# Optimization experiments

Measured on AMD Instinct MI355X. Metric: run time of the kernel, lower is better.

## Reference

```python
import jax, jax.numpy as jnp
import numpy as np

B, T, N, H, E, K, HOR, OD = 64, 12, 1024, 64, 16, 3, 12, 1
DIN = 1  # input_dim
EPS = 1e-12


def setup_inputs() -> dict:
    key = jax.random.key(0)
    ks = jax.random.split(key, 8)
    s = 0.02
    return {
        "source": jax.random.normal(ks[0], (B, T, N, DIN), jnp.float32),
        "node_emb": jax.random.normal(ks[1], (N, E), jnp.float32),
        "time_emb": jax.random.normal(ks[2], (T, E), jnp.float32),
        "gate_wp": jax.random.normal(ks[3], (E, K, DIN + H, 2 * H), jnp.float32) * s,
        "gate_bp": jax.random.normal(ks[4], (E, 2 * H), jnp.float32) * s,
        "gate_lng": jnp.ones((E,), jnp.float32),
        "gate_lnb": jnp.zeros((E,), jnp.float32),
        "upd_wp": jax.random.normal(ks[5], (E, K, DIN + H, H), jnp.float32) * s,
        "upd_bp": jax.random.normal(ks[6], (E, H), jnp.float32) * s,
        "upd_lng": jnp.ones((E,), jnp.float32),
        "upd_lnb": jnp.zeros((E,), jnp.float32),
        "out_lng": jnp.ones((H,), jnp.float32),
        "out_lnb": jnp.zeros((H,), jnp.float32),
        "conv_w": jax.random.normal(ks[7], (HOR * OD, H), jnp.float32) * s,
        "conv_b": jnp.zeros((HOR * OD,), jnp.float32),
    }


def _ln(x, g, b):
    m = x.mean(-1, keepdims=True)
    v = x.var(-1, keepdims=True)
    return (x - m) / jnp.sqrt(v + EPS) * g + b


def _dagcn(x, node_emb, t_emb, wp, bp, lng, lnb):
    # x: [B, N, C]; node_emb: [N, E]; t_emb: [E] (one timestep)
    e = _ln(node_emb + t_emb[None, :], lng, lnb)          # [N, E] (dropout off in eval)
    sup = jax.nn.softmax(e @ e.T, axis=1)                  # [N, N]
    sl = [jnp.eye(N, dtype=x.dtype), sup]
    for _ in range(2, K):
        sl.append(2.0 * sup @ sl[-1] - sl[-2])             # Chebyshev recursion
    S = jnp.stack(sl, axis=0)                              # [K, N, N]
    w = jnp.einsum('nd,dkio->nkio', e, wp)                 # per-node weights
    bias = e @ bp                                          # [N, O]
    xg = jnp.einsum('knm,bmc->bnkc', S, x)                 # graph conv
    return jnp.einsum('bnki,nkio->bno', xg, w) + bias


def reference(source, node_emb, time_emb, gate_wp, gate_bp, gate_lng, gate_lnb,
              upd_wp, upd_bp, upd_lng, upd_lnb, out_lng, out_lnb, conv_w, conv_b):
    def step(state, xs):
        x_t, te = xs                                        # [B,N,DIN], [E]
        zr = jax.nn.sigmoid(_dagcn(jnp.concatenate([x_t, state], -1),
                                   node_emb, te, gate_wp, gate_bp, gate_lng, gate_lnb))
        z, r = zr[..., :H], zr[..., H:]
        hc = jnp.tanh(_dagcn(jnp.concatenate([x_t, z * state], -1),
                             node_emb, te, upd_wp, upd_bp, upd_lng, upd_lnb))
        h = r * state + (1.0 - r) * hc
        return h, None

    xs = jnp.swapaxes(source, 0, 1)                        # [T,B,N,DIN]
    h0 = jnp.zeros((B, N, H), source.dtype)
    h, _ = jax.lax.scan(step, h0, (xs, time_emb))          # last hidden state [B,N,H]
    y = _ln(h, out_lng, out_lnb)                           # out_dropout off in eval
    out = jnp.einsum('bnh,oh->bon', y, conv_w) + conv_b[None, :, None]  # end_conv
    return out.reshape(B, HOR, OD, N).transpose(0, 1, 3, 2)  # [B,horizon,N,output_dim]
```

## Files before the change

### kernel.cpp

```cpp
#include <hip/hip_runtime.h>
#include <math.h>

namespace {
constexpr int B_ = 64, T_ = 12, N_ = 1024, H_ = 64, E_ = 16;
constexpr int C_  = 65;
constexpr int BC_ = B_ * C_;
constexpr int OG_ = 128;
constexpr int OU_ = 64;
constexpr float EPS_ = 1e-12f;
constexpr int KP_ = 224;
constexpr int COLG_ = OG_ * KP_;
constexpr int COLU_ = OU_ * KP_;
constexpr int NE_ = N_ * E_;
}

typedef unsigned short u16;
typedef unsigned int u32;
using f16x8 = __attribute__((ext_vector_type(8))) _Float16;
using f16x4 = __attribute__((ext_vector_type(4))) _Float16;
using f32x4 = __attribute__((ext_vector_type(4))) float;

__device__ __forceinline__ u32 div65(u32 x) { return (x * 16135u) >> 20; }

__device__ __forceinline__ void gl_lds16(const void* g, void* l, int lane) {
#if __has_builtin(__builtin_amdgcn_global_load_lds)
  __builtin_amdgcn_global_load_lds((const __attribute__((address_space(1))) u32*)g,
                                   (__attribute__((address_space(3))) u32*)l, 16, 0, 0);
#else
  *(uint4*)((char*)l + lane * 16) = *(const uint4*)g;
#endif
}

__device__ __forceinline__ void wprep_body(const float* __restrict__ wp, int NO,
                                           _Float16* __restrict__ wpC, int k, int tid) {
  if (tid >= NO) return;
  f16x8 lo = {}, hi = {};
  if (k < 195) {
    const u32 seg = div65((u32)k);
    const u32 ii = k - seg * 65;
#pragma unroll
    for (int d = 0; d < 8; d++)
      lo[d] = (_Float16)wp[(((size_t)d * 3 + seg) * 65 + ii) * NO + tid];
#pragma unroll
    for (int d = 0; d < 8; d++)
      hi[d] = (_Float16)wp[(((size_t)(d + 8) * 3 + seg) * 65 + ii) * NO + tid];
  }
  _Float16* dst = &wpC[((size_t)tid * KP_ + k) * 16];
  *(f16x8*)dst = lo;
  *(f16x8*)(dst + 8) = hi;
}

__device__ __forceinline__ void sup_body(const float* __restrict__ eT,
                                         _Float16* __restrict__ s16,
                                         int n, int tid, float* red) {
  float en[E_];
#pragma unroll
  for (int d = 0; d < E_; d++) en[d] = eT[d * N_ + n];
  float lg[4];
  float mx = -3.4e38f;
#pragma unroll
  for (int j = 0; j < 4; j++) {
    int m = tid + 256 * j;
    float s = 0.f;
#pragma unroll
    for (int d = 0; d < E_; d++) s = fmaf(en[d], eT[d * N_ + m], s);
    lg[j] = s;
    mx = fmaxf(mx, s);
  }
  red[tid] = mx; __syncthreads();
  for (int off = 128; off > 0; off >>= 1) {
    if (tid < off) red[tid] = fmaxf(red[tid], red[tid + off]);
    __syncthreads();
  }
  mx = red[0]; __syncthreads();
  float sum = 0.f;
#pragma unroll
  for (int j = 0; j < 4; j++) { lg[j] = __expf(lg[j] - mx); sum += lg[j]; }
  red[tid] = sum; __syncthreads();
  for (int off = 128; off > 0; off >>= 1) {
    if (tid < off) red[tid] += red[tid + off];
    __syncthreads();
  }
  float inv = 1.0f / red[0];
#pragma unroll
  for (int j = 0; j < 4; j++)
    s16[(size_t)n * N_ + tid + 256 * j] = (_Float16)(lg[j] * inv);
}

__device__ __forceinline__ void wgen_body(const float* __restrict__ e,
                                          const _Float16* __restrict__ wpC, int COLS,
                                          _Float16* __restrict__ Wt,
                                          int xb, int yb, int tid, float (*es)[16]) {
  const int col0 = xb * 1024 + tid * 4;
  const int n0 = yb * 64;
#pragma unroll
  for (int q = 0; q < 4; q++) {
    int idx = tid + q * 256;
    es[idx >> 4][idx & 15] = e[(size_t)n0 * 16 + idx];
  }
  __syncthreads();
  float wc[4][16];
#pragma unroll
  for (int cc = 0; cc < 4; cc++) {
    f16x8 a = *(const f16x8*)&wpC[(size_t)(col0 + cc) * 16];
    f16x8 b = *(const f16x8*)&wpC[(size_t)(col0 + cc) * 16 + 8];
#pragma unroll
    for (int d = 0; d < 8; d++) { wc[cc][d] = (float)a[d]; wc[cc][8 + d] = (float)b[d]; }
  }
  for (int nn = 0; nn < 64; nn++) {
    float acc[4] = {};
#pragma unroll
    for (int d = 0; d < 16; d++) {
      float ev = es[nn][d];
#pragma unroll
      for (int cc = 0; cc < 4; cc++) acc[cc] = fmaf(ev, wc[cc][d], acc[cc]);
    }
    f16x4 pv;
#pragma unroll
    for (int cc = 0; cc < 4; cc++) pv[cc] = (_Float16)acc[cc];
    *(f16x4*)&Wt[(size_t)(n0 + nn) * COLS + col0] = pv;
  }
}

__device__ __forceinline__ void supT_body(const _Float16* __restrict__ S,
                                          _Float16* __restrict__ ST,
                                          int tile, int tid, _Float16 (*lds)[66]) {
  const int n0 = (tile >> 4) * 64;
  const int m0 = (tile & 15) * 64;
  {
    const int r = tid >> 2, c0 = (tid & 3) * 16;
    const _Float16* sp = &S[(size_t)(n0 + r) * 1024 + m0 + c0];
    f16x8 a = *(const f16x8*)sp;
    f16x8 b = *(const f16x8*)(sp + 8);
#pragma unroll
    for (int i = 0; i < 8; i++) { lds[r][c0 + i] = a[i]; lds[r][c0 + 8 + i] = b[i]; }
  }
  __syncthreads();
  {
    const int c = tid >> 2, r0 = (tid & 3) * 16;
    f16x8 a, b;
#pragma unroll
    for (int i = 0; i < 8; i++) { a[i] = lds[r0 + i][c]; b[i] = lds[r0 + 8 + i][c]; }
    _Float16* dp = &ST[(size_t)(m0 + c) * 1024 + n0 + r0];
    *(f16x8*)dp = a;
    *(f16x8*)(dp + 8) = b;
  }
}

__device__ __forceinline__ void gemm_body(
    const _Float16* __restrict__ A, const _Float16* __restrict__ Bt,
    _Float16* __restrict__ rowout,
    int bx, int by, int tid, _Float16* As, _Float16* Bs) {
  const int wave = tid >> 6, lane = tid & 63;
  const int m0 = by * 128, c0 = bx * 64;
  const int lrow = lane >> 3;
  const int lchunk = lane & 7;
  const int fm = lane & 15, fq = lane >> 4;
  f32x4 acc[2][4] = {};
  for (int ks = 0; ks < 16; ks++) {
    const int kp = ks * 64;
#pragma unroll
    for (int q = 0; q < 4; q++) {
      const int seg = wave * 4 + q;
      const int row = seg * 8 + lrow;
      const int sw = lchunk ^ (row & 7);
      gl_lds16(A + (size_t)(m0 + row) * 1024 + kp + sw * 8, &As[seg * 8 * 64], lane);
    }
#pragma unroll
    for (int q = 0; q < 2; q++) {
      const int seg = wave * 2 + q;
      const int row = seg * 8 + lrow;
      const int sw = lchunk ^ (row & 7);
      gl_lds16(Bt + (size_t)(c0 + row) * 1024 + kp + sw * 8, &Bs[seg * 8 * 64], lane);
    }
    __syncthreads();
#pragma unroll
    for (int kk = 0; kk < 2; kk++) {
      f16x8 af[2], bfr[4];
      const int g = kk * 4 + fq;
#pragma unroll
      for (int mt = 0; mt < 2; mt++) {
        const int row = wave * 32 + mt * 16 + fm;
        af[mt] = *(const f16x8*)&As[row * 64 + (g ^ (row & 7)) * 8];
      }
#pragma unroll
      for (int nt = 0; nt < 4; nt++) {
        const int row = nt * 16 + fm;
        bfr[nt] = *(const f16x8*)&Bs[row * 64 + (g ^ (row & 7)) * 8];
      }
#pragma unroll
      for (int mt = 0; mt < 2; mt++)
#pragma unroll
        for (int nt = 0; nt < 4; nt++)
          acc[mt][nt] = __builtin_amdgcn_mfma_f32_16x16x32_f16(af[mt], bfr[nt], acc[mt][nt], 0, 0, 0);
    }
    __syncthreads();
  }
  const int q4 = fq * 4;
#pragma unroll
  for (int nt = 0; nt < 4; nt++) {
    const int col = c0 + nt * 16 + fm;
#pragma unroll
    for (int mt = 0; mt < 2; mt++) {
      const int row = m0 + wave * 32 + mt * 16 + q4;
      const f32x4 v = acc[mt][nt];
#pragma unroll
      for (int j = 0; j < 4; j++)
        rowout[(size_t)(row + j) * 1024 + col] = (_Float16)v[j];
    }
  }
}

__device__ __forceinline__ void gemm2_body(
    const _Float16* __restrict__ A1, const _Float16* __restrict__ A2,
    const _Float16* __restrict__ Bt, _Float16* xg,
    int bx, int by, int tid,
    _Float16* As1, _Float16* As2, _Float16* Bs) {
  const int wave = tid >> 6, lane = tid & 63;
  const int m0 = by * 128, c0 = bx * 64;
  const int lrow = lane >> 3;
  const int lchunk = lane & 7;
  const int fm = lane & 15, fq = lane >> 4;
  f32x4 acc1[2][4] = {}, acc2[2][4] = {};
  for (int ks = 0; ks < 16; ks++) {
    const int kp = ks * 64;
#pragma unroll
    for (int q = 0; q < 4; q++) {
      const int seg = wave * 4 + q;
      const int row = seg * 8 + lrow;
      const int sw = lchunk ^ (row & 7);
      const size_t go = (size_t)(m0 + row) * 1024 + kp + sw * 8;
      gl_lds16(A1 + go, &As1[seg * 8 * 64], lane);
      gl_lds16(A2 + go, &As2[seg * 8 * 64], lane);
    }
#pragma unroll
    for (int q = 0; q < 2; q++) {
      const int seg = wave * 2 + q;
      const int row = seg * 8 + lrow;
      const int sw = lchunk ^ (row & 7);
      gl_lds16(Bt + (size_t)(c0 + row) * 1024 + kp + sw * 8, &Bs[seg * 8 * 64], lane);
    }
    __syncthreads();
#pragma unroll
    for (int kk = 0; kk < 2; kk++) {
      f16x8 a1[2], a2[2], bfr[4];
      const int g = kk * 4 + fq;
#pragma unroll
      for (int mt = 0; mt < 2; mt++) {
        const int row = wave * 32 + mt * 16 + fm;
        const int o = row * 64 + (g ^ (row & 7)) * 8;
        a1[mt] = *(const f16x8*)&As1[o];
        a2[mt] = *(const f16x8*)&As2[o];
      }
#pragma unroll
      for (int nt = 0; nt < 4; nt++) {
        const int row = nt * 16 + fm;
        bfr[nt] = *(const f16x8*)&Bs[row * 64 + (g ^ (row & 7)) * 8];
      }
#pragma unroll
      for (int mt = 0; mt < 2; mt++)
#pragma unroll
        for (int nt = 0; nt < 4; nt++) {
          acc1[mt][nt] = __builtin_amdgcn_mfma_f32_16x16x32_f16(a1[mt], bfr[nt], acc1[mt][nt], 0, 0, 0);
          acc2[mt][nt] = __builtin_amdgcn_mfma_f32_16x16x32_f16(a2[mt], bfr[nt], acc2[mt][nt], 0, 0, 0);
        }
    }
    __syncthreads();
  }
  const int q4 = fq * 4;
#pragma unroll
  for (int nt = 0; nt < 4; nt++) {
    const int col = c0 + nt * 16 + fm;
    if (col >= BC_) continue;
    const u32 bq = div65((u32)col), cq = (u32)col - bq * 65;
#pragma unroll
    for (int mt = 0; mt < 2; mt++) {
      const int row = m0 + wave * 32 + mt * 16 + q4;
      const f32x4 v1 = acc1[mt][nt];
      const f32x4 v2 = acc2[mt][nt];
#pragma unroll
      for (int j = 0; j < 4; j++) {
        size_t base = ((size_t)(row + j) * 64 + bq) * KP_;
        xg[base + 65 + cq] = (_Float16)v1[j];
        xg[base + 130 + cq] = (_Float16)(2.f * v2[j] - (float)xg[base + cq]);
      }
    }
  }
}

__global__ __launch_bounds__(256) void k_pre0(
    const float* __restrict__ gate_wp, const float* __restrict__ upd_wp,
    _Float16* __restrict__ wpCg, _Float16* __restrict__ wpCu,
    const float* __restrict__ node_emb, const float* __restrict__ time_emb,
    const float* __restrict__ g_lng, const float* __restrict__ g_lnb,
    const float* __restrict__ u_lng, const float* __restrict__ u_lnb,
    float* __restrict__ eg_all, float* __restrict__ egT_all,
    float* __restrict__ eu_all, float* __restrict__ euT_all) {
  const int bid = blockIdx.x, tid = threadIdx.x;
  if (bid < KP_)     { wprep_body(gate_wp, OG_, wpCg, bid, tid); return; }
  if (bid < 2 * KP_) { wprep_body(upd_wp,  OU_, wpCu, bid - KP_, tid); return; }
  const int idx = bid - 2 * KP_;
  const int t = idx >> 2;
  const int n = (idx & 3) * 256 + tid;
  float v[E_];
  float m = 0.f;
#pragma unroll
  for (int d = 0; d < E_; d++) { v[d] = node_emb[n * E_ + d] + time_emb[t * E_ + d]; m += v[d]; }
  m *= (1.0f / E_);
  float var = 0.f;
#pragma unroll
  for (int d = 0; d < E_; d++) { float x = v[d] - m; var += x * x; }
  var *= (1.0f / E_);
  float rs = rsqrtf(var + EPS_);
#pragma unroll
  for (int d = 0; d < E_; d++) {
    float nv = (v[d] - m) * rs;
    float g = nv * g_lng[d] + g_lnb[d];
    float u = nv * u_lng[d] + u_lnb[d];
    eg_all[(size_t)t * NE_ + n * E_ + d] = g;
    egT_all[(size_t)t * NE_ + d * N_ + n] = g;
    eu_all[(size_t)t * NE_ + n * E_ + d] = u;
    euT_all[(size_t)t * NE_ + d * N_ + n] = u;
  }
}

__global__ __launch_bounds__(256) void k_pro(
    const float* __restrict__ egT0, const float* __restrict__ euT0,
    const float* __restrict__ src,
    _Float16* __restrict__ supG, _Float16* __restrict__ supU0,
    _Float16* __restrict__ Xt, _Float16* __restrict__ xg) {
  __shared__ float red[256];
  const int bid = blockIdx.x, tid = threadIdx.x;
  if (bid < 1024) { sup_body(egT0, supG, bid, tid, red); return; }
  if (bid < 2048) { sup_body(euT0, supU0, bid - 1024, tid, red); return; }
  const int idx = bid - 2048;
  const int b = idx & 63, m0 = (idx >> 6) * 64;
  for (int q = 0; q < 17; q++) {
    int i = tid + q * 256;
    if (i < 64 * 65) {
      int c = i >> 6, m = i & 63;
      float xv = (c == 0) ? src[((size_t)b * T_) * N_ + m0 + m] : 0.f;
      Xt[((size_t)(b * C_ + c)) * 1024 + m0 + m] = (_Float16)xv;
      u32 mm = div65((u32)i), cc = (u32)i - mm * 65;
      float xv2 = (cc == 0) ? src[((size_t)b * T_) * N_ + m0 + mm] : 0.f;
      xg[((size_t)(m0 + mm) * 64 + b) * KP_ + cc] = (_Float16)xv2;
    }
  }
#pragma unroll
  for (int q = 0; q < 8; q++) {
    int i = tid + q * 256;
    int mm = i >> 5, kk = 192 + (i & 31);
    xg[((size_t)(m0 + mm) * 64 + b) * KP_ + kk] = (_Float16)0.f;
  }
}

__global__ __launch_bounds__(256) void k_proT(
    const _Float16* __restrict__ supG0, const _Float16* __restrict__ supU0,
    _Float16* __restrict__ supGT, _Float16* __restrict__ supUT) {
  __shared__ _Float16 lds[64][66];
  const int bid = blockIdx.x;
  if (bid < 256) supT_body(supG0, supGT, bid, threadIdx.x, lds);
  else           supT_body(supU0, supUT, bid - 256, threadIdx.x, lds);
}

__global__ __launch_bounds__(256) void k_pro2(
    const _Float16* __restrict__ supG0, const _Float16* __restrict__ supGT,
    const _Float16* __restrict__ supU0, const _Float16* __restrict__ supUT,
    _Float16* __restrict__ sup2G0, _Float16* __restrict__ sup2U0) {
  __shared__ __align__(16) _Float16 smem[12288];
  const int bid = blockIdx.x, tid = threadIdx.x;
  if (bid < 128)
    gemm_body(supG0, supGT, sup2G0, bid % 16, bid / 16, tid, smem, smem + 8192);
  else
    gemm_body(supU0, supUT, sup2U0, (bid - 128) % 16, (bid - 128) / 16, tid, smem, smem + 8192);
}

__global__ __launch_bounds__(256) void k_tr(const _Float16* __restrict__ xg,
                                            _Float16* __restrict__ Xt) {
  __shared__ _Float16 tile[64][66];
  const int b = blockIdx.x & 63, m0 = (blockIdx.x >> 6) * 64;
  const int tid = threadIdx.x;
  {
    const int m = tid >> 2, c4 = tid & 3;
    const _Float16* rp = &xg[((size_t)(m0 + m) * 64 + b) * KP_ + c4 * 16];
    f16x8 v0 = *(const f16x8*)rp;
    f16x8 v1 = *(const f16x8*)(rp + 8);
#pragma unroll
    for (int i = 0; i < 8; i++) {
      tile[m][c4 * 16 + i] = v0[i];
      tile[m][c4 * 16 + 8 + i] = v1[i];
    }
    if (c4 == 0) tile[m][64] = rp[64];
  }
  __syncthreads();
  {
    const int m = tid & 63, cg = tid >> 6;
    for (int cc = cg; cc < 65; cc += 4)
      Xt[((size_t)(b * C_ + cc)) * 1024 + m0 + m] = tile[m][cc];
  }
}

__global__ __launch_bounds__(256) void k_ga(
    const _Float16* __restrict__ supG_t, const _Float16* __restrict__ sup2G_t,
    const _Float16* __restrict__ Xt, _Float16* xg,
    const float* __restrict__ eg_t, const _Float16* __restrict__ wpCg,
    _Float16* __restrict__ WtG,
    const float* __restrict__ egT_nx, const float* __restrict__ euT_nx,
    _Float16* __restrict__ supG_nx, _Float16* __restrict__ supU_nx) {
  __shared__ __align__(16) _Float16 smem[20480];
  const int bid = blockIdx.x, tid = threadIdx.x;
  if (bid < 528) {
    gemm2_body(supG_t, sup2G_t, Xt, xg, bid % 66, bid / 66, tid,
               smem, smem + 8192, smem + 16384);
  } else if (bid < 976) {
    const int w = bid - 528;
    wgen_body(eg_t, wpCg, COLG_, WtG, w % 28, w / 28, tid, (float(*)[16])smem);
  } else if (bid < 2000) {
    sup_body(egT_nx, supG_nx, bid - 976, tid, (float*)smem);
  } else {
    sup_body(euT_nx, supU_nx, bid - 2000, tid, (float*)smem);
  }
}

__global__ __launch_bounds__(256) void k_cgT(
    const float* __restrict__ eg, const _Float16* XG,
    const _Float16* __restrict__ Wt, const float* __restrict__ bp,
    const _Float16* __restrict__ h16, const float* __restrict__ src, int t,
    _Float16* __restrict__ r16, _Float16* xgo,
    const _Float16* __restrict__ supG_nx, const _Float16* __restrict__ supU_nx,
    _Float16* __restrict__ supGT, _Float16* __restrict__ supUT) {
  __shared__ __align__(16) char smraw[19456];
  const int bid = blockIdx.x;
  const int tid = threadIdx.x;
  if (bid >= 1024) {
    _Float16 (*lds)[66] = (_Float16(*)[66])smraw;
    if (bid < 1280) supT_body(supG_nx, supGT, bid - 1024, tid, lds);
    else            supT_body(supU_nx, supUT, bid - 1280, tid, lds);
    return;
  }
  float* es = (float*)smraw;
  float* bias_s = (float*)(smraw + 64);
  _Float16 (*zs)[72] = (_Float16(*)[72])(smraw + 576);
  _Float16 (*rs)[72] = (_Float16(*)[72])(smraw + 9792);
  const int n = bid;
  const int wave = tid >> 6, lane = tid & 63;
  const int fm = lane & 15, fq = lane >> 4;
  const int wm = wave >> 1, wn = wave & 1;
  if (tid < 16) es[tid] = eg[n * 16 + tid];
  __syncthreads();
  if (tid < 128) {
    float bv = 0.f;
#pragma unroll
    for (int d = 0; d < 16; d++) bv = fmaf(es[d], bp[d * OG_ + tid], bv);
    bias_s[tid] = bv;
  }
  const _Float16* Ab = XG + (size_t)n * 64 * KP_;
  const _Float16* Bb = Wt + (size_t)n * OG_ * KP_;
  f16x8 af[2][2], bf[2][4];
#pragma unroll
  for (int mt = 0; mt < 2; mt++)
    af[0][mt] = *(const f16x8*)&Ab[(wm * 32 + mt * 16 + fm) * KP_ + fq * 8];
#pragma unroll
  for (int nt = 0; nt < 4; nt++)
    bf[0][nt] = *(const f16x8*)&Bb[(wn * 64 + nt * 16 + fm) * KP_ + fq * 8];
  f32x4 acc[2][4] = {};
#pragma unroll
  for (int kk = 0; kk < 7; kk++) {
    const int cur = kk & 1;
    if (kk < 6) {
      const int ko = (kk + 1) * 32 + fq * 8;
#pragma unroll
      for (int mt = 0; mt < 2; mt++)
        af[cur ^ 1][mt] = *(const f16x8*)&Ab[(wm * 32 + mt * 16 + fm) * KP_ + ko];
#pragma unroll
      for (int nt = 0; nt < 4; nt++)
        bf[cur ^ 1][nt] = *(const f16x8*)&Bb[(wn * 64 + nt * 16 + fm) * KP_ + ko];
    }
#pragma unroll
    for (int mt = 0; mt < 2; mt++)
#pragma unroll
      for (int nt = 0; nt < 4; nt++)
        acc[mt][nt] = __builtin_amdgcn_mfma_f32_16x16x32_f16(af[cur][mt], bf[cur][nt], acc[mt][nt], 0, 0, 0);
  }
  __syncthreads();
#pragma unroll
  for (int nt = 0; nt < 4; nt++) {
    const int o = wn * 64 + nt * 16 + fm;
    const float bias = bias_s[o];
#pragma unroll
    for (int mt = 0; mt < 2; mt++) {
      const f32x4 v = acc[mt][nt];
#pragma unroll
      for (int j = 0; j < 4; j++) {
        const int b = wm * 32 + mt * 16 + fq * 4 + j;
        float s = 1.0f / (1.0f + __expf(-(v[j] + bias)));
        if (wn == 0) zs[b][o] = (_Float16)s;
        else         rs[b][o - H_] = (_Float16)s;
      }
    }
  }
  __syncthreads();
  {
    const int b = tid >> 2, q = tid & 3;
    const _Float16* hp = &h16[((size_t)b * N_ + n) * H_ + q * 16];
    _Float16* xp = &xgo[((size_t)n * 64 + b) * KP_ + 1 + q * 16];
    _Float16* rp = &r16[((size_t)b * N_ + n) * H_ + q * 16];
    f16x8 r0, r1;
#pragma unroll
    for (int i = 0; i < 8; i++) {
      r0[i] = rs[b][q * 16 + i];
      r1[i] = rs[b][q * 16 + 8 + i];
    }
    *(f16x8*)rp = r0;
    *(f16x8*)(rp + 8) = r1;
    f16x8 h0 = *(const f16x8*)hp;
    f16x8 h1 = *(const f16x8*)(hp + 8);
    f16x8 x0, x1;
#pragma unroll
    for (int i = 0; i < 8; i++) {
      x0[i] = (_Float16)((float)zs[b][q * 16 + i] * (float)h0[i]);
      x1[i] = (_Float16)((float)zs[b][q * 16 + 8 + i] * (float)h1[i]);
    }
    *(f16x8*)xp = x0;
    *(f16x8*)(xp + 8) = x1;
    if (tid < 64) {
      float sv = src[((size_t)tid * T_ + t) * N_ + n];
      xgo[((size_t)n * 64 + tid) * KP_] = (_Float16)sv;
    }
  }
}

__global__ __launch_bounds__(256) void k_gu(
    const _Float16* __restrict__ supU_t, const _Float16* __restrict__ sup2U_t,
    const _Float16* __restrict__ Xt, _Float16* xg,
    const float* __restrict__ eu_t, const _Float16* __restrict__ wpCu,
    _Float16* __restrict__ WtU,
    const _Float16* __restrict__ supG_nx, const _Float16* __restrict__ supGT,
    const _Float16* __restrict__ supU_nx, const _Float16* __restrict__ supUT,
    _Float16* __restrict__ sup2G_nx, _Float16* __restrict__ sup2U_nx) {
  __shared__ __align__(16) _Float16 smem[20480];
  const int bid = blockIdx.x, tid = threadIdx.x;
  if (bid < 528) {
    gemm2_body(supU_t, sup2U_t, Xt, xg, bid % 66, bid / 66, tid,
               smem, smem + 8192, smem + 16384);
  } else if (bid < 752) {
    const int w = bid - 528;
    wgen_body(eu_t, wpCu, COLU_, WtU, w % 14, w / 14, tid, (float(*)[16])smem);
  } else if (bid < 880) {
    const int w = bid - 752;
    gemm_body(supG_nx, supGT, sup2G_nx, w % 16, w / 16, tid, smem, smem + 8192);
  } else {
    const int w = bid - 880;
    gemm_body(supU_nx, supUT, sup2U_nx, w % 16, w / 16, tid, smem, smem + 8192);
  }
}

__global__ __launch_bounds__(256) void k_cu(
    const float* __restrict__ eu, const _Float16* XG,
    const _Float16* __restrict__ Wt, const float* __restrict__ bp,
    const _Float16* __restrict__ r16, const float* __restrict__ src,
    int t, int donext,
    _Float16* __restrict__ h16, _Float16* xgo) {
  const int n = blockIdx.x;
  const int tid = threadIdx.x;
  const int wave = tid >> 6, lane = tid & 63;
  const int fm = lane & 15, fq = lane >> 4;
  __shared__ float es[16];
  __shared__ float bias_s[64];
  __shared__ _Float16 hs[64][72];
  __shared__ _Float16 rs[64][72];
  if (tid < 16) es[tid] = eu[n * 16 + tid];
  __syncthreads();
  if (tid < 64) {
    float bv = 0.f;
#pragma unroll
    for (int d = 0; d < 16; d++) bv = fmaf(es[d], bp[d * OU_ + tid], bv);
    bias_s[tid] = bv;
  }
  {
    const int b = tid >> 2, q = tid & 3;
    const _Float16* hp = &h16[((size_t)b * N_ + n) * H_ + q * 16];
    const _Float16* rp = &r16[((size_t)b * N_ + n) * H_ + q * 16];
    f16x8 h0 = *(const f16x8*)hp;
    f16x8 h1 = *(const f16x8*)(hp + 8);
    f16x8 r0 = *(const f16x8*)rp;
    f16x8 r1 = *(const f16x8*)(rp + 8);
#pragma unroll
    for (int i = 0; i < 8; i++) {
      hs[b][q * 16 + i] = h0[i];
      hs[b][q * 16 + 8 + i] = h1[i];
      rs[b][q * 16 + i] = r0[i];
      rs[b][q * 16 + 8 + i] = r1[i];
    }
  }
  __syncthreads();
  const _Float16* Ab = XG + (size_t)n * 64 * KP_;
  const _Float16* Bb = Wt + (size_t)n * OU_ * KP_;
  f16x8 af[2], bf[2][4];
  af[0] = *(const f16x8*)&Ab[(wave * 16 + fm) * KP_ + fq * 8];
#pragma unroll
  for (int nt = 0; nt < 4; nt++)
    bf[0][nt] = *(const f16x8*)&Bb[(nt * 16 + fm) * KP_ + fq * 8];
  f32x4 acc[4] = {};
#pragma unroll
  for (int kk = 0; kk < 7; kk++) {
    const int cur = kk & 1;
    if (kk < 6) {
      const int ko = (kk + 1) * 32 + fq * 8;
      af[cur ^ 1] = *(const f16x8*)&Ab[(wave * 16 + fm) * KP_ + ko];
#pragma unroll
      for (int nt = 0; nt < 4; nt++)
        bf[cur ^ 1][nt] = *(const f16x8*)&Bb[(nt * 16 + fm) * KP_ + ko];
    }
#pragma unroll
    for (int nt = 0; nt < 4; nt++)
      acc[nt] = __builtin_amdgcn_mfma_f32_16x16x32_f16(af[cur], bf[cur][nt], acc[nt], 0, 0, 0);
  }
#pragma unroll
  for (int nt = 0; nt < 4; nt++) {
    const int o = nt * 16 + fm;
    const float bias = bias_s[o];
    const f32x4 v = acc[nt];
#pragma unroll
    for (int j = 0; j < 4; j++) {
      const int b = wave * 16 + fq * 4 + j;
      float hc = tanhf(v[j] + bias);
      float rv = (float)rs[b][o];
      float hv = (float)hs[b][o];
      hs[b][o] = (_Float16)(rv * hv + (1.0f - rv) * hc);
    }
  }
  __syncthreads();
  {
    const int b = tid >> 2, q = tid & 3;
    _Float16* hp = &h16[((size_t)b * N_ + n) * H_ + q * 16];
    f16x8 h0, h1;
#pragma unroll
    for (int i = 0; i < 8; i++) {
      h0[i] = hs[b][q * 16 + i];
      h1[i] = hs[b][q * 16 + 8 + i];
    }
    *(f16x8*)hp = h0;
    *(f16x8*)(hp + 8) = h1;
    if (donext) {
      _Float16* xp = &xgo[((size_t)n * 64 + b) * KP_ + 1 + q * 16];
      *(f16x8*)xp = h0;
      *(f16x8*)(xp + 8) = h1;
      if (tid < 64) {
        float sv = src[((size_t)tid * T_ + (t + 1)) * N_ + n];
        xgo[((size_t)n * 64 + tid) * KP_] = (_Float16)sv;
      }
    }
  }
}

__global__ __launch_bounds__(256) void k_final(const _Float16* __restrict__ h16,
                                               const float* __restrict__ out_lng,
                                               const float* __restrict__ out_lnb,
                                               const float* __restrict__ conv_w,
                                               const float* __restrict__ conv_b,
                                               float* __restrict__ out) {
  const int b = blockIdx.x >> 2;
  const int n = (blockIdx.x & 3) * 256 + threadIdx.x;
  __shared__ float cw[12][64];
  __shared__ float cb[12];
  __shared__ float lgs[64], lbs[64];
  for (int idx = threadIdx.x; idx < 12 * 64; idx += 256) cw[idx >> 6][idx & 63] = conv_w[idx];
  if (threadIdx.x < 12) cb[threadIdx.x] = conv_b[threadIdx.x];
  if (threadIdx.x < 64) { lgs[threadIdx.x] = out_lng[threadIdx.x]; lbs[threadIdx.x] = out_lnb[threadIdx.x]; }
  __syncthreads();
  const _Float16* hp = &h16[((size_t)b * N_ + n) * H_];
  float hv[64];
  float mean = 0.f;
#pragma unroll
  for (int i8 = 0; i8 < 8; i8++) {
    f16x8 v = *(const f16x8*)&hp[i8 * 8];
#pragma unroll
    for (int j = 0; j < 8; j++) { hv[i8 * 8 + j] = (float)v[j]; mean += hv[i8 * 8 + j]; }
  }
  mean *= (1.0f / H_);
  float var = 0.f;
#pragma unroll
  for (int i = 0; i < 64; i++) { float d = hv[i] - mean; var += d * d; }
  var *= (1.0f / H_);
  const float rs = rsqrtf(var + EPS_);
  float y[64];
#pragma unroll
  for (int i = 0; i < 64; i++)
    y[i] = (hv[i] - mean) * rs * lgs[i] + lbs[i];
#pragma unroll
  for (int o = 0; o < 12; o++) {
    float acc = cb[o];
#pragma unroll
    for (int i = 0; i < 64; i++) acc = fmaf(y[i], cw[o][i], acc);
    out[((size_t)b * 12 + o) * N_ + n] = acc;
  }
}

extern "C" void kernel_launch(void* const* d_in, const int* in_sizes, int n_in,
                              void* d_out, int out_size, void* d_ws, size_t ws_size,
                              hipStream_t stream) {
  const float* src      = (const float*)d_in[0];
  const float* node_emb = (const float*)d_in[1];
  const float* time_emb = (const float*)d_in[2];
  const float* gate_wp  = (const float*)d_in[3];
  const float* gate_bp  = (const float*)d_in[4];
  const float* gate_lng = (const float*)d_in[5];
  const float* gate_lnb = (const float*)d_in[6];
  const float* upd_wp   = (const float*)d_in[7];
  const float* upd_bp   = (const float*)d_in[8];
  const float* upd_lng  = (const float*)d_in[9];
  const float* upd_lnb  = (const float*)d_in[10];
  const float* out_lng  = (const float*)d_in[11];
  const float* out_lnb  = (const float*)d_in[12];
  const float* conv_w   = (const float*)d_in[13];
  const float* conv_b   = (const float*)d_in[14];
  float* out = (float*)d_out;

  constexpr size_t SZ_H16 = (size_t)B_ * N_ * H_ / 2;
  constexpr size_t SZ_R   = SZ_H16;
  constexpr size_t SZ_T   = (size_t)BC_ * 1024 / 2;
  constexpr size_t SZ_XG  = (size_t)N_ * 64 * KP_ / 2;
  constexpr size_t SZ_WT  = (size_t)N_ * OG_ * KP_ / 2;
  constexpr size_t SZ_WCG = (size_t)COLG_ * 16 / 2;
  constexpr size_t SZ_WCU = (size_t)COLU_ * 16 / 2;
  constexpr size_t SZ_S   = (size_t)N_ * N_ / 2;

  float* ws = (float*)d_ws;
  size_t off = 0;
  float* h16F   = ws + off; off += SZ_H16;
  float* r16F   = ws + off; off += SZ_R;
  float* XtF    = ws + off; off += SZ_T;
  float* xgF    = ws + off; off += SZ_XG;
  float* WtF    = ws + off; off += SZ_WT;
  float* wcgF   = ws + off; off += SZ_WCG;
  float* wcuF   = ws + off; off += SZ_WCU;
  float* supGF  = ws + off; off += 2 * SZ_S;
  float* supUF  = ws + off; off += 2 * SZ_S;
  float* supGTF = ws + off; off += SZ_S;
  float* supUTF = ws + off; off += SZ_S;
  float* s2GF   = ws + off; off += 2 * SZ_S;
  float* s2UF   = ws + off; off += 2 * SZ_S;
  float* eg_all  = ws + off; off += (size_t)T_ * NE_;
  float* egT_all = ws + off; off += (size_t)T_ * NE_;
  float* eu_all  = ws + off; off += (size_t)T_ * NE_;
  float* euT_all = ws + off; off += (size_t)T_ * NE_;
  if (ws_size < off * sizeof(float)) return;

  _Float16* h16   = (_Float16*)h16F;
  _Float16* r16   = (_Float16*)r16F;
  _Float16* Xt    = (_Float16*)XtF;
  _Float16* xg    = (_Float16*)xgF;
  _Float16* WtG   = (_Float16*)WtF;
  _Float16* WtU   = (_Float16*)WtF;
  _Float16* wpCg  = (_Float16*)wcgF;
  _Float16* wpCu  = (_Float16*)wcuF;
  _Float16* supG  = (_Float16*)supGF;
  _Float16* supU  = (_Float16*)supUF;
  _Float16* supGT = (_Float16*)supGTF;
  _Float16* supUT = (_Float16*)supUTF;
  _Float16* s2G   = (_Float16*)s2GF;
  _Float16* s2U   = (_Float16*)s2UF;
  const size_t SB = (size_t)N_ * N_;

  hipMemsetAsync(h16, 0, SZ_H16 * sizeof(float), stream);
  k_pre0<<<2 * KP_ + 48, 256, 0, stream>>>(gate_wp, upd_wp, wpCg, wpCu,
                                           node_emb, time_emb,
                                           gate_lng, gate_lnb, upd_lng, upd_lnb,
                                           eg_all, egT_all, eu_all, euT_all);
  k_pro<<<3072, 256, 0, stream>>>(egT_all, euT_all, src, supG, supU, Xt, xg);
  k_proT<<<512, 256, 0, stream>>>(supG, supU, supGT, supUT);
  k_pro2<<<256, 256, 0, stream>>>(supG, supGT, supU, supUT, s2G, s2U);

  for (int t = 0; t < T_; t++) {
    const int cur = t & 1, nxt = (t + 1) & 1;
    _Float16* supG_t  = supG + (size_t)cur * SB;
    _Float16* supG_nx = supG + (size_t)nxt * SB;
    _Float16* supU_t  = supU + (size_t)cur * SB;
    _Float16* supU_nx = supU + (size_t)nxt * SB;
    _Float16* s2G_t   = s2G + (size_t)cur * SB;
    _Float16* s2G_nx  = s2G + (size_t)nxt * SB;
    _Float16* s2U_t   = s2U + (size_t)cur * SB;
    _Float16* s2U_nx  = s2U + (size_t)nxt * SB;
    const float* eg_t = eg_all + (size_t)t * NE_;
    const float* eu_t = eu_all + (size_t)t * NE_;
    const int more = (t < T_ - 1) ? 1 : 0;
    const int tn = more ? t + 1 : t;

    k_ga<<<more ? 3024 : 976, 256, 0, stream>>>(
        supG_t, s2G_t, Xt, xg, eg_t, wpCg, WtG,
        egT_all + (size_t)tn * NE_, euT_all + (size_t)tn * NE_, supG_nx, supU_nx);
    k_cgT<<<more ? 1536 : 1024, 256, 0, stream>>>(
        eg_t, xg, WtG, gate_bp, h16, src, t, r16, xg,
        supG_nx, supU_nx, supGT, supUT);
    k_tr<<<1024, 256, 0, stream>>>(xg, Xt);
    k_gu<<<more ? 1008 : 752, 256, 0, stream>>>(
        supU_t, s2U_t, Xt, xg, eu_t, wpCu, WtU,
        supG_nx, supGT, supU_nx, supUT, s2G_nx, s2U_nx);
    k_cu<<<N_, 256, 0, stream>>>(eu_t, xg, WtU, upd_bp, r16, src, t, more, h16, xg);
    if (more) k_tr<<<1024, 256, 0, stream>>>(xg, Xt);
  }
  k_final<<<B_ * N_ / 256, 256, 0, stream>>>(h16, out_lng, out_lnb, conv_w, conv_b, out);
}
```

Measured before the change: 2.098 ms.

## Split xg into contiguous row buffers and stage per-node operand in LDS

The graph-conv GEMM epilogue now writes its two outputs to contiguous row-major buffers (node x B*65) instead of scattering into a padded per-node KP layout, and no longer reads x0 back for the Chebyshev term. The consumer kernels k_cgT and k_cu assemble the [64 x 232] operand in shared memory, computing 2*y2 - x0 and zero padding there, then run the MFMA loop from LDS. k_tr is rewritten to transpose from the contiguous X0 rows with vectorized stores. The intent is coalesced epilogue writes and no read-modify-write in the GEMM. In exchange it costs extra LDS, a staging pass, and loses the register double-buffering of the A operand.

```diff
diff --git a/kernel.cpp b/kernel.cpp
--- a/kernel.cpp
+++ b/kernel.cpp
@@ -5,10 +5,12 @@
 constexpr int B_ = 64, T_ = 12, N_ = 1024, H_ = 64, E_ = 16;
 constexpr int C_  = 65;
 constexpr int BC_ = B_ * C_;
+constexpr int NPAD_ = 4224;
 constexpr int OG_ = 128;
 constexpr int OU_ = 64;
 constexpr float EPS_ = 1e-12f;
 constexpr int KP_ = 224;
+constexpr int KS_ = 232;
 constexpr int COLG_ = OG_ * KP_;
 constexpr int COLU_ = OU_ * KP_;
 constexpr int NE_ = N_ * E_;
@@ -21,6 +23,7 @@
 using f32x4 = __attribute__((ext_vector_type(4))) float;
 
 __device__ __forceinline__ u32 div65(u32 x) { return (x * 16135u) >> 20; }
+__device__ __forceinline__ u32 div29(u32 x) { return (x * 565u) >> 14; }
 
 __device__ __forceinline__ void gl_lds16(const void* g, void* l, int lane) {
 #if __has_builtin(__builtin_amdgcn_global_load_lds)
@@ -213,7 +216,8 @@
 
 __device__ __forceinline__ void gemm2_body(
     const _Float16* __restrict__ A1, const _Float16* __restrict__ A2,
-    const _Float16* __restrict__ Bt, _Float16* xg,
+    const _Float16* __restrict__ Bt,
+    _Float16* __restrict__ y1row, _Float16* __restrict__ y2row,
     int bx, int by, int tid,
     _Float16* As1, _Float16* As2, _Float16* Bs) {
   const int wave = tid >> 6, lane = tid & 63;
@@ -272,7 +276,6 @@
   for (int nt = 0; nt < 4; nt++) {
     const int col = c0 + nt * 16 + fm;
     if (col >= BC_) continue;
-    const u32 bq = div65((u32)col), cq = (u32)col - bq * 65;
 #pragma unroll
     for (int mt = 0; mt < 2; mt++) {
       const int row = m0 + wave * 32 + mt * 16 + q4;
@@ -280,11 +283,31 @@
       const f32x4 v2 = acc2[mt][nt];
 #pragma unroll
       for (int j = 0; j < 4; j++) {
-        size_t base = ((size_t)(row + j) * 64 + bq) * KP_;
-        xg[base + 65 + cq] = (_Float16)v1[j];
-        xg[base + 130 + cq] = (_Float16)(2.f * v2[j] - (float)xg[base + cq]);
+        y1row[(size_t)(row + j) * BC_ + col] = (_Float16)v1[j];
+        y2row[(size_t)(row + j) * BC_ + col] = (_Float16)v2[j];
       }
     }
+  }
+}
+
+__device__ __forceinline__ void stage_xg(
+    const _Float16* __restrict__ x0p, const _Float16* __restrict__ y1p,
+    const _Float16* __restrict__ y2p, int tid, _Float16* __restrict__ XGs) {
+  for (int idx = tid; idx < BC_; idx += 256) {
+    const u32 b = div65((u32)idx), k = (u32)idx - b * 65;
+    XGs[b * KS_ + k] = x0p[idx];
+  }
+  for (int idx = tid; idx < BC_; idx += 256) {
+    const u32 b = div65((u32)idx), k = (u32)idx - b * 65;
+    XGs[b * KS_ + 65 + k] = y1p[idx];
+  }
+  for (int idx = tid; idx < BC_; idx += 256) {
+    const u32 b = div65((u32)idx), k = (u32)idx - b * 65;
+    XGs[b * KS_ + 130 + k] = (_Float16)(2.f * (float)y2p[idx] - (float)x0p[idx]);
+  }
+  for (int idx = tid; idx < 64 * 29; idx += 256) {
+    const u32 b = div29((u32)idx), k = (u32)idx - b * 29;
+    XGs[b * KS_ + 195 + k] = (_Float16)0.f;
   }
 }
 
@@ -328,7 +351,7 @@
     const float* __restrict__ egT0, const float* __restrict__ euT0,
     const float* __restrict__ src,
     _Float16* __restrict__ supG, _Float16* __restrict__ supU0,
-    _Float16* __restrict__ Xt, _Float16* __restrict__ xg) {
+    _Float16* __restrict__ Xt, _Float16* __restrict__ X0row) {
   __shared__ float red[256];
   const int bid = blockIdx.x, tid = threadIdx.x;
   if (bid < 1024) { sup_body(egT0, supG, bid, tid, red); return; }
@@ -343,14 +366,8 @@
       Xt[((size_t)(b * C_ + c)) * 1024 + m0 + m] = (_Float16)xv;
       u32 mm = div65((u32)i), cc = (u32)i - mm * 65;
       float xv2 = (cc == 0) ? src[((size_t)b * T_) * N_ + m0 + mm] : 0.f;
-      xg[((size_t)(m0 + mm) * 64 + b) * KP_ + cc] = (_Float16)xv2;
-    }
-  }
-#pragma unroll
-  for (int q = 0; q < 8; q++) {
-    int i = tid + q * 256;
-    int mm = i >> 5, kk = 192 + (i & 31);
-    xg[((size_t)(m0 + mm) * 64 + b) * KP_ + kk] = (_Float16)0.f;
+      X0row[((size_t)(m0 + mm)) * BC_ + b * 65 + cc] = (_Float16)xv2;
+    }
   }
 }
 
@@ -375,34 +392,34 @@
     gemm_body(supU0, supUT, sup2U0, (bid - 128) % 16, (bid - 128) / 16, tid, smem, smem + 8192);
 }
 
-__global__ __launch_bounds__(256) void k_tr(const _Float16* __restrict__ xg,
+__global__ __launch_bounds__(256) void k_tr(const _Float16* __restrict__ X0,
                                             _Float16* __restrict__ Xt) {
   __shared__ _Float16 tile[64][66];
-  const int b = blockIdx.x & 63, m0 = (blockIdx.x >> 6) * 64;
+  const int c0 = (blockIdx.x % 65) * 64;
+  const int m0 = (blockIdx.x / 65) * 64;
   const int tid = threadIdx.x;
+#pragma unroll
+  for (int q = 0; q < 16; q++) {
+    int idx = tid + q * 256;
+    int m = idx >> 6, c = idx & 63;
+    tile[m][c] = X0[(size_t)(m0 + m) * BC_ + c0 + c];
+  }
+  __syncthreads();
   {
-    const int m = tid >> 2, c4 = tid & 3;
-    const _Float16* rp = &xg[((size_t)(m0 + m) * 64 + b) * KP_ + c4 * 16];
-    f16x8 v0 = *(const f16x8*)rp;
-    f16x8 v1 = *(const f16x8*)(rp + 8);
-#pragma unroll
-    for (int i = 0; i < 8; i++) {
-      tile[m][c4 * 16 + i] = v0[i];
-      tile[m][c4 * 16 + 8 + i] = v1[i];
-    }
-    if (c4 == 0) tile[m][64] = rp[64];
-  }
-  __syncthreads();
-  {
-    const int m = tid & 63, cg = tid >> 6;
-    for (int cc = cg; cc < 65; cc += 4)
-      Xt[((size_t)(b * C_ + cc)) * 1024 + m0 + m] = tile[m][cc];
+    const int c = tid >> 2, mq = (tid & 3) * 16;
+    f16x8 a, b;
+#pragma unroll
+    for (int i = 0; i < 8; i++) { a[i] = tile[mq + i][c]; b[i] = tile[mq + 8 + i][c]; }
+    _Float16* dp = &Xt[(size_t)(c0 + c) * 1024 + m0 + mq];
+    *(f16x8*)dp = a;
+    *(f16x8*)(dp + 8) = b;
   }
 }
 
 __global__ __launch_bounds__(256) void k_ga(
     const _Float16* __restrict__ supG_t, const _Float16* __restrict__ sup2G_t,
-    const _Float16* __restrict__ Xt, _Float16* xg,
+    const _Float16* __restrict__ Xt,
+    _Float16* __restrict__ y1row, _Float16* __restrict__ y2row,
     const float* __restrict__ eg_t, const _Float16* __restrict__ wpCg,
     _Float16* __restrict__ WtG,
     const float* __restrict__ egT_nx, const float* __restrict__ euT_nx,
@@ -410,7 +427,7 @@
   __shared__ __align__(16) _Float16 smem[20480];
   const int bid = blockIdx.x, tid = threadIdx.x;
   if (bid < 528) {
-    gemm2_body(supG_t, sup2G_t, Xt, xg, bid % 66, bid / 66, tid,
+    gemm2_body(supG_t, sup2G_t, Xt, y1row, y2row, bid % 66, bid / 66, tid,
                smem, smem + 8192, smem + 16384);
   } else if (bid < 976) {
     const int w = bid - 528;
@@ -423,13 +440,15 @@
 }
 
 __global__ __launch_bounds__(256) void k_cgT(
-    const float* __restrict__ eg, const _Float16* XG,
+    const float* __restrict__ eg,
+    const _Float16* __restrict__ X0, const _Float16* __restrict__ y1r,
+    const _Float16* __restrict__ y2r,
     const _Float16* __restrict__ Wt, const float* __restrict__ bp,
     const _Float16* __restrict__ h16, const float* __restrict__ src, int t,
-    _Float16* __restrict__ r16, _Float16* xgo,
+    _Float16* __restrict__ r16, _Float16* X0out,
     const _Float16* __restrict__ supG_nx, const _Float16* __restrict__ supU_nx,
     _Float16* __restrict__ supGT, _Float16* __restrict__ supUT) {
-  __shared__ __align__(16) char smraw[19456];
+  __shared__ __align__(16) char smraw[30272];
   const int bid = blockIdx.x;
   const int tid = threadIdx.x;
   if (bid >= 1024) {
@@ -440,6 +459,7 @@
   }
   float* es = (float*)smraw;
   float* bias_s = (float*)(smraw + 64);
+  _Float16* XGs = (_Float16*)(smraw + 576);
   _Float16 (*zs)[72] = (_Float16(*)[72])(smraw + 576);
   _Float16 (*rs)[72] = (_Float16(*)[72])(smraw + 9792);
   const int n = bid;
@@ -447,6 +467,7 @@
   const int fm = lane & 15, fq = lane >> 4;
   const int wm = wave >> 1, wn = wave & 1;
   if (tid < 16) es[tid] = eg[n * 16 + tid];
+  stage_xg(X0 + (size_t)n * BC_, y1r + (size_t)n * BC_, y2r + (size_t)n * BC_, tid, XGs);
   __syncthreads();
   if (tid < 128) {
     float bv = 0.f;
@@ -454,33 +475,23 @@
     for (int d = 0; d < 16; d++) bv = fmaf(es[d], bp[d * OG_ + tid], bv);
     bias_s[tid] = bv;
   }
-  const _Float16* Ab = XG + (size_t)n * 64 * KP_;
   const _Float16* Bb = Wt + (size_t)n * OG_ * KP_;
-  f16x8 af[2][2], bf[2][4];
-#pragma unroll
-  for (int mt = 0; mt < 2; mt++)
-    af[0][mt] = *(const f16x8*)&Ab[(wm * 32 + mt * 16 + fm) * KP_ + fq * 8];
-#pragma unroll
-  for (int nt = 0; nt < 4; nt++)
-    bf[0][nt] = *(const f16x8*)&Bb[(wn * 64 + nt * 16 + fm) * KP_ + fq * 8];
   f32x4 acc[2][4] = {};
 #pragma unroll
   for (int kk = 0; kk < 7; kk++) {
-    const int cur = kk & 1;
-    if (kk < 6) {
-      const int ko = (kk + 1) * 32 + fq * 8;
-#pragma unroll
-      for (int mt = 0; mt < 2; mt++)
-        af[cur ^ 1][mt] = *(const f16x8*)&Ab[(wm * 32 + mt * 16 + fm) * KP_ + ko];
+    const int ko = kk * 32 + fq * 8;
+    f16x8 af[2], bf[4];
+#pragma unroll
+    for (int mt = 0; mt < 2; mt++)
+      af[mt] = *(const f16x8*)&XGs[(wm * 32 + mt * 16 + fm) * KS_ + ko];
+#pragma unroll
+    for (int nt = 0; nt < 4; nt++)
+      bf[nt] = *(const f16x8*)&Bb[(wn * 64 + nt * 16 + fm) * KP_ + ko];
+#pragma unroll
+    for (int mt = 0; mt < 2; mt++)
 #pragma unroll
       for (int nt = 0; nt < 4; nt++)
-        bf[cur ^ 1][nt] = *(const f16x8*)&Bb[(wn * 64 + nt * 16 + fm) * KP_ + ko];
-    }
-#pragma unroll
-    for (int mt = 0; mt < 2; mt++)
-#pragma unroll
-      for (int nt = 0; nt < 4; nt++)
-        acc[mt][nt] = __builtin_amdgcn_mfma_f32_16x16x32_f16(af[cur][mt], bf[cur][nt], acc[mt][nt], 0, 0, 0);
+        acc[mt][nt] = __builtin_amdgcn_mfma_f32_16x16x32_f16(af[mt], bf[nt], acc[mt][nt], 0, 0, 0);
   }
   __syncthreads();
 #pragma unroll
@@ -503,7 +514,7 @@
   {
     const int b = tid >> 2, q = tid & 3;
     const _Float16* hp = &h16[((size_t)b * N_ + n) * H_ + q * 16];
-    _Float16* xp = &xgo[((size_t)n * 64 + b) * KP_ + 1 + q * 16];
+    _Float16* xp = &X0out[(size_t)n * BC_ + b * 65 + 1 + q * 16];
     _Float16* rp = &r16[((size_t)b * N_ + n) * H_ + q * 16];
     f16x8 r0, r1;
 #pragma unroll
@@ -525,14 +536,15 @@
     *(f16x8*)(xp + 8) = x1;
     if (tid < 64) {
       float sv = src[((size_t)tid * T_ + t) * N_ + n];
-      xgo[((size_t)n * 64 + tid) * KP_] = (_Float16)sv;
+      X0out[(size_t)n * BC_ + tid * 65] = (_Float16)sv;
     }
   }
 }
 
 __global__ __launch_bounds__(256) void k_gu(
     const _Float16* __restrict__ supU_t, const _Float16* __restrict__ sup2U_t,
-    const _Float16* __restrict__ Xt, _Float16* xg,
+    const _Float16* __restrict__ Xt,
+    _Float16* __restrict__ y1row, _Float16* __restrict__ y2row,
     const float* __restrict__ eu_t, const _Float16* __restrict__ wpCu,
     _Float16* __restrict__ WtU,
     const _Float16* __restrict__ supG_nx, const _Float16* __restrict__ supGT,
@@ -541,7 +553,7 @@
   __shared__ __align__(16) _Float16 smem[20480];
   const int bid = blockIdx.x, tid = threadIdx.x;
   if (bid < 528) {
-    gemm2_body(supU_t, sup2U_t, Xt, xg, bid % 66, bid / 66, tid,
+    gemm2_body(supU_t, sup2U_t, Xt, y1row, y2row, bid % 66, bid / 66, tid,
                smem, smem + 8192, smem + 16384);
   } else if (bid < 752) {
     const int w = bid - 528;
@@ -556,20 +568,25 @@
 }
 
 __global__ __launch_bounds__(256) void k_cu(
-    const float* __restrict__ eu, const _Float16* XG,
+    const float* __restrict__ eu,
+    const _Float16* __restrict__ X0, const _Float16* __restrict__ y1r,
+    const _Float16* __restrict__ y2r,
     const _Float16* __restrict__ Wt, const float* __restrict__ bp,
     const _Float16* __restrict__ r16, const float* __restrict__ src,
     int t, int donext,
-    _Float16* __restrict__ h16, _Float16* xgo) {
+    _Float16* __restrict__ h16, _Float16* X0out) {
+  __shared__ __align__(16) char smraw[30016];
+  float* es = (float*)smraw;
+  float* bias_s = (float*)(smraw + 64);
+  _Float16* XGs = (_Float16*)(smraw + 320);
+  _Float16 (*hs)[72] = (_Float16(*)[72])(smraw + 320);
+  _Float16 (*rs)[72] = (_Float16(*)[72])(smraw + 9536);
   const int n = blockIdx.x;
   const int tid = threadIdx.x;
   const int wave = tid >> 6, lane = tid & 63;
   const int fm = lane & 15, fq = lane >> 4;
-  __shared__ float es[16];
-  __shared__ float bias_s[64];
-  __shared__ _Float16 hs[64][72];
-  __shared__ _Float16 rs[64][72];
   if (tid < 16) es[tid] = eu[n * 16 + tid];
+  stage_xg(X0 + (size_t)n * BC_, y1r + (size_t)n * BC_, y2r + (size_t)n * BC_, tid, XGs);
   __syncthreads();
   if (tid < 64) {
     float bv = 0.f;
@@ -577,6 +594,21 @@
     for (int d = 0; d < 16; d++) bv = fmaf(es[d], bp[d * OU_ + tid], bv);
     bias_s[tid] = bv;
   }
+  const _Float16* Bb = Wt + (size_t)n * OU_ * KP_;
+  f32x4 acc[4] = {};
+#pragma unroll
+  for (int kk = 0; kk < 7; kk++) {
+    const int ko = kk * 32 + fq * 8;
+    f16x8 af = *(const f16x8*)&XGs[(wave * 16 + fm) * KS_ + ko];
+    f16x8 bf[4];
+#pragma unroll
+    for (int nt = 0; nt < 4; nt++)
+      bf[nt] = *(const f16x8*)&Bb[(nt * 16 + fm) * KP_ + ko];
+#pragma unroll
+    for (int nt = 0; nt < 4; nt++)
+      acc[nt] = __builtin_amdgcn_mfma_f32_16x16x32_f16(af, bf[nt], acc[nt], 0, 0, 0);
+  }
+  __syncthreads();
   {
     const int b = tid >> 2, q = tid & 3;
     const _Float16* hp = &h16[((size_t)b * N_ + n) * H_ + q * 16];
@@ -594,28 +626,6 @@
     }
   }
   __syncthreads();
-  const _Float16* Ab = XG + (size_t)n * 64 * KP_;
-  const _Float16* Bb = Wt + (size_t)n * OU_ * KP_;
-  f16x8 af[2], bf[2][4];
-  af[0] = *(const f16x8*)&Ab[(wave * 16 + fm) * KP_ + fq * 8];
-#pragma unroll
-  for (int nt = 0; nt < 4; nt++)
-    bf[0][nt] = *(const f16x8*)&Bb[(nt * 16 + fm) * KP_ + fq * 8];
-  f32x4 acc[4] = {};
-#pragma unroll
-  for (int kk = 0; kk < 7; kk++) {
-    const int cur = kk & 1;
-    if (kk < 6) {
-      const int ko = (kk + 1) * 32 + fq * 8;
-      af[cur ^ 1] = *(const f16x8*)&Ab[(wave * 16 + fm) * KP_ + ko];
-#pragma unroll
-      for (int nt = 0; nt < 4; nt++)
-        bf[cur ^ 1][nt] = *(const f16x8*)&Bb[(nt * 16 + fm) * KP_ + ko];
-    }
-#pragma unroll
-    for (int nt = 0; nt < 4; nt++)
-      acc[nt] = __builtin_amdgcn_mfma_f32_16x16x32_f16(af[cur], bf[cur][nt], acc[nt], 0, 0, 0);
-  }
 #pragma unroll
   for (int nt = 0; nt < 4; nt++) {
     const int o = nt * 16 + fm;
@@ -643,12 +653,12 @@
     *(f16x8*)hp = h0;
     *(f16x8*)(hp + 8) = h1;
     if (donext) {
-      _Float16* xp = &xgo[((size_t)n * 64 + b) * KP_ + 1 + q * 16];
+      _Float16* xp = &X0out[(size_t)n * BC_ + b * 65 + 1 + q * 16];
       *(f16x8*)xp = h0;
       *(f16x8*)(xp + 8) = h1;
       if (tid < 64) {
         float sv = src[((size_t)tid * T_ + (t + 1)) * N_ + n];
-        xgo[((size_t)n * 64 + tid) * KP_] = (_Float16)sv;
+        X0out[(size_t)n * BC_ + tid * 65] = (_Float16)sv;
       }
     }
   }
@@ -719,8 +729,8 @@
 
   constexpr size_t SZ_H16 = (size_t)B_ * N_ * H_ / 2;
   constexpr size_t SZ_R   = SZ_H16;
-  constexpr size_t SZ_T   = (size_t)BC_ * 1024 / 2;
-  constexpr size_t SZ_XG  = (size_t)N_ * 64 * KP_ / 2;
+  constexpr size_t SZ_T   = (size_t)NPAD_ * 1024 / 2;
+  constexpr size_t SZ_ROW = (size_t)N_ * BC_ / 2;
   constexpr size_t SZ_WT  = (size_t)N_ * OG_ * KP_ / 2;
   constexpr size_t SZ_WCG = (size_t)COLG_ * 16 / 2;
   constexpr size_t SZ_WCU = (size_t)COLU_ * 16 / 2;
@@ -731,7 +741,9 @@
   float* h16F   = ws + off; off += SZ_H16;
   float* r16F   = ws + off; off += SZ_R;
   float* XtF    = ws + off; off += SZ_T;
-  float* xgF    = ws + off; off += SZ_XG;
+  float* X0F    = ws + off; off += SZ_ROW;
+  float* y1F    = ws + off; off += SZ_ROW;
+  float* y2F    = ws + off; off += SZ_ROW;
   float* WtF    = ws + off; off += SZ_WT;
   float* wcgF   = ws + off; off += SZ_WCG;
   float* wcuF   = ws + off; off += SZ_WCU;
@@ -750,7 +762,9 @@
   _Float16* h16   = (_Float16*)h16F;
   _Float16* r16   = (_Float16*)r16F;
   _Float16* Xt    = (_Float16*)XtF;
-  _Float16* xg    = (_Float16*)xgF;
+  _Float16* X0row = (_Float16*)X0F;
+  _Float16* y1row = (_Float16*)y1F;
+  _Float16* y2row = (_Float16*)y2F;
   _Float16* WtG   = (_Float16*)WtF;
   _Float16* WtU   = (_Float16*)WtF;
   _Float16* wpCg  = (_Float16*)wcgF;
@@ -768,7 +782,7 @@
                                            node_emb, time_emb,
                                            gate_lng, gate_lnb, upd_lng, upd_lnb,
                                            eg_all, egT_all, eu_all, euT_all);
-  k_pro<<<3072, 256, 0, stream>>>(egT_all, euT_all, src, supG, supU, Xt, xg);
+  k_pro<<<3072, 256, 0, stream>>>(egT_all, euT_all, src, supG, supU, Xt, X0row);
   k_proT<<<512, 256, 0, stream>>>(supG, supU, supGT, supUT);
   k_pro2<<<256, 256, 0, stream>>>(supG, supGT, supU, supUT, s2G, s2U);
 
@@ -788,17 +802,18 @@
     const int tn = more ? t + 1 : t;
 
     k_ga<<<more ? 3024 : 976, 256, 0, stream>>>(
-        supG_t, s2G_t, Xt, xg, eg_t, wpCg, WtG,
+        supG_t, s2G_t, Xt, y1row, y2row, eg_t, wpCg, WtG,
         egT_all + (size_t)tn * NE_, euT_all + (size_t)tn * NE_, supG_nx, supU_nx);
     k_cgT<<<more ? 1536 : 1024, 256, 0, stream>>>(
-        eg_t, xg, WtG, gate_bp, h16, src, t, r16, xg,
+        eg_t, X0row, y1row, y2row, WtG, gate_bp, h16, src, t, r16, X0row,
         supG_nx, supU_nx, supGT, supUT);
-    k_tr<<<1024, 256, 0, stream>>>(xg, Xt);
+    k_tr<<<1040, 256, 0, stream>>>(X0row, Xt);
     k_gu<<<more ? 1008 : 752, 256, 0, stream>>>(
-        supU_t, s2U_t, Xt, xg, eu_t, wpCu, WtU,
+        supU_t, s2U_t, Xt, y1row, y2row, eu_t, wpCu, WtU,
         supG_nx, supGT, supU_nx, supUT, s2G_nx, s2U_nx);
-    k_cu<<<N_, 256, 0, stream>>>(eu_t, xg, WtU, upd_bp, r16, src, t, more, h16, xg);
-    if (more) k_tr<<<1024, 256, 0, stream>>>(xg, Xt);
+    k_cu<<<N_, 256, 0, stream>>>(eu_t, X0row, y1row, y2row, WtU, upd_bp, r16,
+                                 src, t, more, h16, X0row);
+    if (more) k_tr<<<1040, 256, 0, stream>>>(X0row, Xt);
   }
   k_final<<<B_ * N_ / 256, 256, 0, stream>>>(h16, out_lng, out_lnb, conv_w, conv_b, out);
 }
```

After: 1.880 ms, median of 2. 10.4% less time.
